# Kernel tuning notes

Hardware: AMD Instinct MI355X
Metric: run time of the kernel (lower is better)

Reference implementation:

```python
import jax, jax.numpy as jnp
import numpy as np

H = 128          # hidden_dim
L = 3            # num_layers
EPS = 1e-5       # BatchNorm eps


def setup_inputs() -> dict:
    key = jax.random.key(0)
    ks = jax.random.split(key, 12)
    B, N = 32, 8192
    s = 0.05
    x = jax.random.normal(ks[0], (B, N, 2), dtype=jnp.float32)
    mask = jnp.ones((B, N), dtype=jnp.float32)
    # parameters, stored as [in, out]
    emb_w = jax.random.normal(ks[1], (2, H), jnp.float32) * s
    emb_b = jnp.zeros((H,), jnp.float32)
    lin_w = jax.random.normal(ks[2], (L, H, H), jnp.float32) * s
    lin_b = jnp.zeros((L, H), jnp.float32)
    nb_w = jax.random.normal(ks[3], (L, H, H), jnp.float32) * s
    nb_b = jnp.zeros((L, H), jnp.float32)
    bn_g = jnp.ones((L, H), jnp.float32)
    bn_b = jnp.zeros((L, H), jnp.float32)
    out1_w = jax.random.normal(ks[4], (H, H // 2), jnp.float32) * s
    out1_b = jnp.zeros((H // 2,), jnp.float32)
    out2_w = jax.random.normal(ks[5], (H // 2, 2), jnp.float32) * s
    out2_b = jnp.zeros((2,), jnp.float32)
    return dict(x=x, mask=mask, emb_w=emb_w, emb_b=emb_b,
                lin_w=lin_w, lin_b=lin_b, nb_w=nb_w, nb_b=nb_b,
                bn_g=bn_g, bn_b=bn_b, out1_w=out1_w, out1_b=out1_b,
                out2_w=out2_w, out2_b=out2_b)


def reference(x, mask, emb_w, emb_b, lin_w, lin_b, nb_w, nb_b,
              bn_g, bn_b, out1_w, out1_b, out2_w, out2_b):
    m = mask[..., None]                     # [B, N, 1]
    h = x @ emb_w + emb_b                   # [B, N, H]
    for i in range(L):
        # graph conv: self transform + ring-neighbor (roll) transform
        nsum = jnp.roll(h, 1, axis=1) + jnp.roll(h, -1, axis=1)
        h_new = (h @ lin_w[i] + lin_b[i] + nsum @ nb_w[i] + nb_b[i]) * m
        # BatchNorm1d (training-mode batch stats over batch*nodes per channel)
        mean = jnp.mean(h_new, axis=(0, 1))
        var = jnp.mean(jnp.square(h_new - mean), axis=(0, 1))  # biased var
        h_new = (h_new - mean) * jax.lax.rsqrt(var + EPS) * bn_g[i] + bn_b[i]
        h_new = jax.nn.relu(h_new)          # dropout treated as identity (eval)
        h = h + h_new                       # residual
    out = jax.nn.relu(h @ out1_w + out1_b) @ out2_w + out2_b  # [B, N, 2]
    return out * m
```

## Files before the change

kernel.cpp:

```cpp
#include <hip/hip_runtime.h>
#include <cstddef>

#define H      128
#define NBATCH 32
#define NN     8192
#define RTOT   (NBATCH*NN)
#define NLAYER 3
#define BNEPS  1e-5f
#define NSLOT  16
#define CNPB   128
#define HNPB   64
#define HS_STRIDE 136

typedef _Float16 f16;
typedef __attribute__((ext_vector_type(8))) _Float16 half8;
typedef __attribute__((ext_vector_type(4))) float f32x4;

__device__ __forceinline__ void unpackh8(uint4 pk, float* d) {
    const f16* hp = (const f16*)&pk;
    #pragma unroll
    for (int i = 0; i < 8; ++i) d[i] = (float)hp[i];
}
__device__ __forceinline__ uint4 packh8(const float* s) {
    uint4 pk;
    f16* hp = (f16*)&pk;
    #pragma unroll
    for (int i = 0; i < 8; ++i) hp[i] = (f16)s[i];
    return pk;
}

__device__ __forceinline__ void load_bfrags(
    const f16* __restrict__ Wt, half8 bW[2][4], int colbase, int l15, int quad)
{
    #pragma unroll
    for (int nt = 0; nt < 2; ++nt) {
        int nrow = colbase + nt * 16 + l15;
        #pragma unroll
        for (int ks = 0; ks < 4; ++ks)
            bW[nt][ks] = *((const half8*)(Wt + nrow * 128 + ks * 32 + quad * 8));
    }
}

__device__ __forceinline__ void conv_mfma8(
    const f16* __restrict__ hs, const half8 bWl[2][4], const half8 bWn[2][4],
    f32x4 acc[8][2], int l15, int quad)
{
    #pragma unroll
    for (int mt = 0; mt < 8; ++mt) {
        acc[mt][0] = (f32x4){0.f, 0.f, 0.f, 0.f};
        acc[mt][1] = (f32x4){0.f, 0.f, 0.f, 0.f};
    }
    #pragma unroll
    for (int ks = 0; ks < 4; ++ks) {
        #pragma unroll
        for (int mt = 0; mt < 8; ++mt) {
            int row = mt * 16 + l15;
            const f16* base = hs + row * HS_STRIDE + ks * 32 + quad * 8;
            half8 hm = *((const half8*)(base + HS_STRIDE));
            half8 hd = *((const half8*)(base));
            half8 hu = *((const half8*)(base + 2 * HS_STRIDE));
            half8 an = hd + hu;
            acc[mt][0] = __builtin_amdgcn_mfma_f32_16x16x32_f16(hm, bWl[0][ks], acc[mt][0], 0, 0, 0);
            acc[mt][1] = __builtin_amdgcn_mfma_f32_16x16x32_f16(hm, bWl[1][ks], acc[mt][1], 0, 0, 0);
            acc[mt][0] = __builtin_amdgcn_mfma_f32_16x16x32_f16(an, bWn[0][ks], acc[mt][0], 0, 0, 0);
            acc[mt][1] = __builtin_amdgcn_mfma_f32_16x16x32_f16(an, bWn[1][ks], acc[mt][1], 0, 0, 0);
        }
    }
}

__global__ __launch_bounds__(256) void k_prep(
    const float* __restrict__ lin_w, const float* __restrict__ nb_w,
    f16* __restrict__ Wlt, f16* __restrict__ Wnt)
{
    int id = blockIdx.x * 256 + threadIdx.x;
    int mat = id / 49152;
    int r   = id - mat * 49152;
    int l   = r >> 14;
    int r2  = r & 16383;
    int k   = r2 >> 7;
    int n   = r2 & 127;
    const float* src = mat ? nb_w : lin_w;
    f16*         dst = mat ? Wnt  : Wlt;
    dst[l * 16384 + n * 128 + k] = (f16)src[l * 16384 + k * 128 + n];
}

__device__ __forceinline__ void conv_epilogue(
    f32x4 acc[8][2], const float bsum[2], const float* __restrict__ msk,
    f16* __restrict__ tr, f16* __restrict__ hnb, float* __restrict__ gstats,
    int r0, int colbase, int l15, int quad, int lane, int t, int slot)
{
    float s[2] = {0.f, 0.f}, ss[2] = {0.f, 0.f};
    #pragma unroll
    for (int nt = 0; nt < 2; ++nt) {
        int col = colbase + nt * 16 + l15;
        #pragma unroll
        for (int mt = 0; mt < 8; ++mt)
            #pragma unroll
            for (int reg = 0; reg < 4; ++reg) {
                int lrow = mt * 16 + quad * 4 + reg;
                float v = (acc[mt][nt][reg] + bsum[nt]) * msk[lrow];
                tr[lrow * HS_STRIDE + col] = (f16)v;
                s[nt] += v; ss[nt] += v * v;
            }
    }
    #pragma unroll
    for (int nt = 0; nt < 2; ++nt) {
        s[nt]  += __shfl_xor(s[nt], 16);  s[nt]  += __shfl_xor(s[nt], 32);
        ss[nt] += __shfl_xor(ss[nt], 16); ss[nt] += __shfl_xor(ss[nt], 32);
    }
    if (lane < 16)
        #pragma unroll
        for (int nt = 0; nt < 2; ++nt) {
            int col = colbase + nt * 16 + lane;
            atomicAdd(&gstats[slot * 2 * H + col],     s[nt]);
            atomicAdd(&gstats[slot * 2 * H + H + col], ss[nt]);
        }
    __syncthreads();
    for (int i = t; i < CNPB * 16; i += 256) {
        int row = i >> 4, g = i & 15;
        *((uint4*)(hnb + (size_t)(r0 + row) * H + g * 8)) =
            *((const uint4*)(tr + row * HS_STRIDE + g * 8));
    }
}

__global__ __launch_bounds__(256) void k_conv0f(
    const float* __restrict__ x, const float* __restrict__ ew,
    const float* __restrict__ eb,
    const f16* __restrict__ Wlt, const f16* __restrict__ Wnt,
    const float* __restrict__ bl, const float* __restrict__ bnb,
    const float* __restrict__ mask,
    f16* __restrict__ hnb, float* __restrict__ gstats)
{
    __shared__ __align__(16) f16 smem[(CNPB + 2) * HS_STRIDE];
    __shared__ float ews[3 * H], msk[CNPB];
    f16* hs = smem;
    f16* tr = smem;
    const int t = threadIdx.x, lane = t & 63;
    const int l15 = lane & 15, quad = lane >> 4;
    const int colbase = (t >> 6) * 32;
    const int r0 = blockIdx.x * CNPB;
    const int batch = r0 >> 13, n0 = r0 & (NN - 1);

    half8 bWl[2][4], bWn[2][4];
    load_bfrags(Wlt, bWl, colbase, l15, quad);
    load_bfrags(Wnt, bWn, colbase, l15, quad);
    float bsum[2];
    #pragma unroll
    for (int nt = 0; nt < 2; ++nt) {
        int col = colbase + nt * 16 + l15;
        bsum[nt] = bl[col] + bnb[col];
    }
    for (int c = t; c < H; c += 256) {
        ews[c] = ew[c]; ews[H + c] = ew[H + c]; ews[2 * H + c] = eb[c];
    }
    if (t < CNPB) msk[t] = mask[r0 + t];
    __syncthreads();

    for (int i = t; i < (CNPB + 2) * 16; i += 256) {
        int row = i >> 4, g = i & 15;
        int n = (n0 + row - 1 + NN) & (NN - 1);
        const float* xp = x + 2 * ((size_t)batch * NN + n);
        float x0 = xp[0], x1 = xp[1];
        f16 o[8];
        #pragma unroll
        for (int e = 0; e < 8; ++e) {
            int c = g * 8 + e;
            o[e] = (f16)fmaf(x1, ews[H + c], fmaf(x0, ews[c], ews[2 * H + c]));
        }
        *((uint4*)(hs + row * HS_STRIDE + g * 8)) = *((const uint4*)o);
    }
    __syncthreads();

    f32x4 acc[8][2];
    conv_mfma8(hs, bWl, bWn, acc, l15, quad);
    __syncthreads();

    conv_epilogue(acc, bsum, msk, tr, hnb, gstats,
                  r0, colbase, l15, quad, lane, t, blockIdx.x & (NSLOT - 1));
}

__global__ __launch_bounds__(256) void k_conv(
    const f16* __restrict__ hb,
    const f16* __restrict__ Wlt, const f16* __restrict__ Wnt,
    const float* __restrict__ bl, const float* __restrict__ bnb,
    const float* __restrict__ mask,
    f16* __restrict__ hnb, float* __restrict__ gstats)
{
    __shared__ __align__(16) f16 smem[(CNPB + 2) * HS_STRIDE];
    __shared__ float msk[CNPB];
    f16* hs = smem;
    f16* tr = smem;
    const int t = threadIdx.x, lane = t & 63;
    const int l15 = lane & 15, quad = lane >> 4;
    const int colbase = (t >> 6) * 32;
    const int r0 = blockIdx.x * CNPB;
    const int batch = r0 >> 13, n0 = r0 & (NN - 1);

    half8 bWl[2][4], bWn[2][4];
    load_bfrags(Wlt, bWl, colbase, l15, quad);
    load_bfrags(Wnt, bWn, colbase, l15, quad);
    float bsum[2];
    #pragma unroll
    for (int nt = 0; nt < 2; ++nt) {
        int col = colbase + nt * 16 + l15;
        bsum[nt] = bl[col] + bnb[col];
    }
    if (t < CNPB) msk[t] = mask[r0 + t];

    for (int i = t; i < (CNPB + 2) * 16; i += 256) {
        int row = i >> 4, g = i & 15;
        int n = (n0 + row - 1 + NN) & (NN - 1);
        *((uint4*)(hs + row * HS_STRIDE + g * 8)) =
            *((const uint4*)(hb + ((size_t)(batch * NN + n)) * H + g * 8));
    }
    __syncthreads();

    f32x4 acc[8][2];
    conv_mfma8(hs, bWl, bWn, acc, l15, quad);
    __syncthreads();

    conv_epilogue(acc, bsum, msk, tr, hnb, gstats,
                  r0, colbase, l15, quad, lane, t, blockIdx.x & (NSLOT - 1));
}

__global__ __launch_bounds__(256) void k_norm0(
    const float* __restrict__ x, const float* __restrict__ ew,
    const float* __restrict__ eb, const f16* __restrict__ hnb,
    const float* __restrict__ gstats, const float* __restrict__ bn_g,
    const float* __restrict__ bn_b, f16* __restrict__ hb)
{
    __shared__ float scl_s[H], sft_s[H], ews[3 * H];
    const int t = threadIdx.x;
    if (t < H) {
        float s = 0.f, ss = 0.f;
        #pragma unroll
        for (int i = 0; i < NSLOT; ++i) {
            s  += gstats[i * 2 * H + t];
            ss += gstats[i * 2 * H + H + t];
        }
        const float invR = 1.f / (float)RTOT;
        float mean = s * invR;
        float var  = ss * invR - mean * mean;
        float inv  = rsqrtf(var + BNEPS);
        float sc   = bn_g[t] * inv;
        scl_s[t] = sc;
        sft_s[t] = fmaf(-mean, sc, bn_b[t]);
        ews[t] = ew[t]; ews[H + t] = ew[H + t]; ews[2 * H + t] = eb[t];
    }
    __syncthreads();

    for (size_t idx = (size_t)blockIdx.x * 256 + t; idx < (size_t)RTOT * 16;
         idx += (size_t)gridDim.x * 256) {
        size_t row = idx >> 4;
        int g = idx & 15;
        float x0 = x[2 * row], x1 = x[2 * row + 1];
        uint4 pn = *((const uint4*)(hnb + row * H + g * 8));
        float vn[8], vh[8];
        unpackh8(pn, vn);
        #pragma unroll
        for (int e = 0; e < 8; ++e) {
            int c = g * 8 + e;
            float h0 = fmaf(x1, ews[H + c], fmaf(x0, ews[c], ews[2 * H + c]));
            vh[e] = h0 + fmaxf(fmaf(vn[e], scl_s[c], sft_s[c]), 0.f);
        }
        *((uint4*)(hb + row * H + g * 8)) = packh8(vh);
    }
}

__global__ __launch_bounds__(256) void k_norm(
    const f16* __restrict__ hnb, const float* __restrict__ gstats,
    const float* __restrict__ bn_g, const float* __restrict__ bn_b,
    f16* __restrict__ hb)
{
    __shared__ float scl_s[H], sft_s[H];
    const int t = threadIdx.x;
    if (t < H) {
        float s = 0.f, ss = 0.f;
        #pragma unroll
        for (int i = 0; i < NSLOT; ++i) {
            s  += gstats[i * 2 * H + t];
            ss += gstats[i * 2 * H + H + t];
        }
        const float invR = 1.f / (float)RTOT;
        float mean = s * invR;
        float var  = ss * invR - mean * mean;
        float inv  = rsqrtf(var + BNEPS);
        float sc   = bn_g[t] * inv;
        scl_s[t] = sc;
        sft_s[t] = fmaf(-mean, sc, bn_b[t]);
    }
    __syncthreads();

    for (size_t idx = (size_t)blockIdx.x * 256 + t; idx < (size_t)RTOT * 16;
         idx += (size_t)gridDim.x * 256) {
        size_t row = idx >> 4;
        int g = idx & 15;
        uint4 pn = *((const uint4*)(hnb + row * H + g * 8));
        uint4 ph = *((const uint4*)(hb  + row * H + g * 8));
        float vn[8], vh[8];
        unpackh8(pn, vn);
        unpackh8(ph, vh);
        #pragma unroll
        for (int e = 0; e < 8; ++e) {
            int c = g * 8 + e;
            vh[e] += fmaxf(fmaf(vn[e], scl_s[c], sft_s[c]), 0.f);
        }
        *((uint4*)(hb + row * H + g * 8)) = packh8(vh);
    }
}

__global__ __launch_bounds__(256) void k_head(
    const f16* __restrict__ hb, const float* __restrict__ W1,
    const float* __restrict__ b1, const float* __restrict__ W2,
    const float* __restrict__ b2, const float* __restrict__ mask,
    float* __restrict__ out)
{
    __shared__ f16 hs [64 * HS_STRIDE];
    __shared__ f16 w1t[64 * HS_STRIDE];
    const int t    = threadIdx.x;
    const int wave = t >> 6;
    const int lane = t & 63;
    const int l15  = lane & 15;
    const int quad = lane >> 4;
    const int r0   = blockIdx.x * HNPB;

    for (int i = t; i < 64 * 16; i += 256) {
        int row = i >> 4, g = i & 15;
        *((uint4*)(hs + row * HS_STRIDE + g * 8)) =
            *((const uint4*)(hb + (size_t)(r0 + row) * H + g * 8));
    }
    for (int i = t; i < H * 64; i += 256) {
        int k = i >> 6, n = i & 63;
        w1t[n * HS_STRIDE + k] = (f16)W1[i];
    }
    __syncthreads();

    f32x4 acc[4];
    #pragma unroll
    for (int nt = 0; nt < 4; ++nt) acc[nt] = (f32x4){0.f, 0.f, 0.f, 0.f};

    #pragma unroll
    for (int ks = 0; ks < 4; ++ks) {
        half8 a = *((const half8*)(hs + (wave * 16 + l15) * HS_STRIDE + ks * 32 + quad * 8));
        #pragma unroll
        for (int nt = 0; nt < 4; ++nt) {
            half8 b = *((const half8*)(w1t + (nt * 16 + l15) * HS_STRIDE + ks * 32 + quad * 8));
            acc[nt] = __builtin_amdgcn_mfma_f32_16x16x32_f16(a, b, acc[nt], 0, 0, 0);
        }
    }

    float p0[4] = {0,0,0,0}, p1[4] = {0,0,0,0};
    #pragma unroll
    for (int nt = 0; nt < 4; ++nt) {
        int col = nt * 16 + l15;
        float bb = b1[col];
        float wa = W2[2 * col], wb = W2[2 * col + 1];
        #pragma unroll
        for (int reg = 0; reg < 4; ++reg) {
            float v = fmaxf(acc[nt][reg] + bb, 0.f);
            p0[reg] = fmaf(v, wa, p0[reg]);
            p1[reg] = fmaf(v, wb, p1[reg]);
        }
    }
    #pragma unroll
    for (int reg = 0; reg < 4; ++reg) {
        p0[reg] += __shfl_xor(p0[reg], 1); p0[reg] += __shfl_xor(p0[reg], 2);
        p0[reg] += __shfl_xor(p0[reg], 4); p0[reg] += __shfl_xor(p0[reg], 8);
        p1[reg] += __shfl_xor(p1[reg], 1); p1[reg] += __shfl_xor(p1[reg], 2);
        p1[reg] += __shfl_xor(p1[reg], 4); p1[reg] += __shfl_xor(p1[reg], 8);
    }
    if (l15 == 0) {
        #pragma unroll
        for (int reg = 0; reg < 4; ++reg) {
            int gr = r0 + wave * 16 + quad * 4 + reg;
            float m = mask[gr];
            float2 o;
            o.x = (p0[reg] + b2[0]) * m;
            o.y = (p1[reg] + b2[1]) * m;
            *((float2*)(out + 2 * gr)) = o;
        }
    }
}

extern "C" void kernel_launch(void* const* d_in, const int* in_sizes, int n_in,
                              void* d_out, int out_size, void* d_ws, size_t ws_size,
                              hipStream_t stream)
{
    const float* x     = (const float*)d_in[0];
    const float* mask  = (const float*)d_in[1];
    const float* emb_w = (const float*)d_in[2];
    const float* emb_b = (const float*)d_in[3];
    const float* lin_w = (const float*)d_in[4];
    const float* lin_b = (const float*)d_in[5];
    const float* nb_w  = (const float*)d_in[6];
    const float* nb_b  = (const float*)d_in[7];
    const float* bn_g  = (const float*)d_in[8];
    const float* bn_b  = (const float*)d_in[9];
    const float* o1w   = (const float*)d_in[10];
    const float* o1b   = (const float*)d_in[11];
    const float* o2w   = (const float*)d_in[12];
    const float* o2b   = (const float*)d_in[13];
    float* out = (float*)d_out;

    char* ws = (char*)d_ws;
    f16* hb  = (f16*)ws;
    f16* hnb = (f16*)(ws + (size_t)RTOT * H * 2);

    float* gst = (float*)d_out;
    f16* Wlt = (f16*)((float*)d_out + 65536);
    f16* Wnt = Wlt + NLAYER * H * H;

    hipMemsetAsync(gst, 0, NLAYER * NSLOT * 2 * H * sizeof(float), stream);
    k_prep<<<384, 256, 0, stream>>>(lin_w, nb_w, Wlt, Wnt);

    k_conv0f<<<RTOT / CNPB, 256, 0, stream>>>(
        x, emb_w, emb_b, Wlt, Wnt, lin_b, nb_b, mask, hnb, gst);
    k_norm0<<<2048, 256, 0, stream>>>(
        x, emb_w, emb_b, hnb, gst, bn_g, bn_b, hb);

    for (int i = 1; i < NLAYER; ++i) {
        k_conv<<<RTOT / CNPB, 256, 0, stream>>>(
            hb, Wlt + i * H * H, Wnt + i * H * H,
            lin_b + i * H, nb_b + i * H, mask,
            hnb, gst + i * NSLOT * 2 * H);
        k_norm<<<2048, 256, 0, stream>>>(
            hnb, gst + i * NSLOT * 2 * H, bn_g + i * H, bn_b + i * H, hb);
    }
    k_head<<<RTOT / HNPB, 256, 0, stream>>>(hb, o1w, o1b, o2w, o2b, mask, out);
}
```

Measured before the change: 352.6 us.

## Store conv output in MFMA fragment order and transpose in norm kernels

The conv epilogue now writes each wave's accumulator fragments straight to global memory in a fragment-native blocked layout. This drops the shared-memory transpose and its two block barriers. The norm kernels now run one block per 128-row tile, read that blocked layout coalesced, apply BN and ReLU, and scatter into shared memory to transpose back to row-major before the residual add. This moves transpose work from the conv kernel to the norm kernel and adds scattered 2-byte LDS stores there, which may cause bank conflicts.

```diff
diff --git a/kernel.cpp b/kernel.cpp
--- a/kernel.cpp
+++ b/kernel.cpp
@@ -84,42 +84,42 @@
     dst[l * 16384 + n * 128 + k] = (f16)src[l * 16384 + k * 128 + n];
 }
 
-__device__ __forceinline__ void conv_epilogue(
+__device__ __forceinline__ void conv_epilogue_c(
     f32x4 acc[8][2], const float bsum[2], const float* __restrict__ msk,
-    f16* __restrict__ tr, f16* __restrict__ hnb, float* __restrict__ gstats,
-    int r0, int colbase, int l15, int quad, int lane, int t, int slot)
-{
+    f16* __restrict__ hnb, float* __restrict__ gstats,
+    int blk, int wave, int quad, int lane, int slot)
+{
+    uint2* out2 = (uint2*)hnb;
     float s[2] = {0.f, 0.f}, ss[2] = {0.f, 0.f};
     #pragma unroll
     for (int nt = 0; nt < 2; ++nt) {
-        int col = colbase + nt * 16 + l15;
-        #pragma unroll
-        for (int mt = 0; mt < 8; ++mt)
+        #pragma unroll
+        for (int mt = 0; mt < 8; ++mt) {
+            f16 v4[4];
             #pragma unroll
             for (int reg = 0; reg < 4; ++reg) {
                 int lrow = mt * 16 + quad * 4 + reg;
                 float v = (acc[mt][nt][reg] + bsum[nt]) * msk[lrow];
-                tr[lrow * HS_STRIDE + col] = (f16)v;
+                v4[reg] = (f16)v;
                 s[nt] += v; ss[nt] += v * v;
             }
+            size_t chunk = ((size_t)blk * 4 + wave) * 16 + mt * 2 + nt;
+            out2[chunk * 64 + lane] = *((const uint2*)v4);
+        }
     }
     #pragma unroll
     for (int nt = 0; nt < 2; ++nt) {
         s[nt]  += __shfl_xor(s[nt], 16);  s[nt]  += __shfl_xor(s[nt], 32);
         ss[nt] += __shfl_xor(ss[nt], 16); ss[nt] += __shfl_xor(ss[nt], 32);
     }
-    if (lane < 16)
+    if (lane < 16) {
+        int colbase = wave * 32;
         #pragma unroll
         for (int nt = 0; nt < 2; ++nt) {
             int col = colbase + nt * 16 + lane;
             atomicAdd(&gstats[slot * 2 * H + col],     s[nt]);
             atomicAdd(&gstats[slot * 2 * H + H + col], ss[nt]);
         }
-    __syncthreads();
-    for (int i = t; i < CNPB * 16; i += 256) {
-        int row = i >> 4, g = i & 15;
-        *((uint4*)(hnb + (size_t)(r0 + row) * H + g * 8)) =
-            *((const uint4*)(tr + row * HS_STRIDE + g * 8));
     }
 }
 
@@ -131,13 +131,12 @@
     const float* __restrict__ mask,
     f16* __restrict__ hnb, float* __restrict__ gstats)
 {
-    __shared__ __align__(16) f16 smem[(CNPB + 2) * HS_STRIDE];
+    __shared__ __align__(16) f16 hs[(CNPB + 2) * HS_STRIDE];
     __shared__ float ews[3 * H], msk[CNPB];
-    f16* hs = smem;
-    f16* tr = smem;
     const int t = threadIdx.x, lane = t & 63;
     const int l15 = lane & 15, quad = lane >> 4;
-    const int colbase = (t >> 6) * 32;
+    const int wave = t >> 6;
+    const int colbase = wave * 32;
     const int r0 = blockIdx.x * CNPB;
     const int batch = r0 >> 13, n0 = r0 & (NN - 1);
 
@@ -173,10 +172,9 @@
 
     f32x4 acc[8][2];
     conv_mfma8(hs, bWl, bWn, acc, l15, quad);
-    __syncthreads();
-
-    conv_epilogue(acc, bsum, msk, tr, hnb, gstats,
-                  r0, colbase, l15, quad, lane, t, blockIdx.x & (NSLOT - 1));
+
+    conv_epilogue_c(acc, bsum, msk, hnb, gstats,
+                    blockIdx.x, wave, quad, lane, blockIdx.x & (NSLOT - 1));
 }
 
 __global__ __launch_bounds__(256) void k_conv(
@@ -186,13 +184,12 @@
     const float* __restrict__ mask,
     f16* __restrict__ hnb, float* __restrict__ gstats)
 {
-    __shared__ __align__(16) f16 smem[(CNPB + 2) * HS_STRIDE];
+    __shared__ __align__(16) f16 hs[(CNPB + 2) * HS_STRIDE];
     __shared__ float msk[CNPB];
-    f16* hs = smem;
-    f16* tr = smem;
     const int t = threadIdx.x, lane = t & 63;
     const int l15 = lane & 15, quad = lane >> 4;
-    const int colbase = (t >> 6) * 32;
+    const int wave = t >> 6;
+    const int colbase = wave * 32;
     const int r0 = blockIdx.x * CNPB;
     const int batch = r0 >> 13, n0 = r0 & (NN - 1);
 
@@ -217,20 +214,42 @@
 
     f32x4 acc[8][2];
     conv_mfma8(hs, bWl, bWn, acc, l15, quad);
-    __syncthreads();
-
-    conv_epilogue(acc, bsum, msk, tr, hnb, gstats,
-                  r0, colbase, l15, quad, lane, t, blockIdx.x & (NSLOT - 1));
-}
-
-__global__ __launch_bounds__(256) void k_norm0(
-    const float* __restrict__ x, const float* __restrict__ ew,
-    const float* __restrict__ eb, const f16* __restrict__ hnb,
+
+    conv_epilogue_c(acc, bsum, msk, hnb, gstats,
+                    blockIdx.x, wave, quad, lane, blockIdx.x & (NSLOT - 1));
+}
+
+__device__ __forceinline__ void norm_ingest(
+    const f16* __restrict__ hnb, int blk, int t,
+    const float* __restrict__ scl_s, const float* __restrict__ sft_s,
+    f16* __restrict__ g)
+{
+    const uint4* src = (const uint4*)hnb + (size_t)blk * 2048;
+    for (int i = t; i < 2048; i += 256) {
+        uint4 pk = src[i];
+        int chunk = i >> 5;
+        int L     = (i & 31) * 2;
+        int ntv   = chunk & 1;
+        int mtv   = (chunk >> 1) & 7;
+        int wv    = chunk >> 4;
+        int c0    = wv * 32 + ntv * 16 + (L & 15);
+        int row0  = mtv * 16 + (L >> 4) * 4;
+        float vv[8];
+        unpackh8(pk, vv);
+        #pragma unroll
+        for (int e = 0; e < 8; ++e) {
+            int cc = c0 + (e >> 2);
+            int rr = row0 + (e & 3);
+            float q = fmaxf(fmaf(vv[e], scl_s[cc], sft_s[cc]), 0.f);
+            g[rr * HS_STRIDE + cc] = (f16)q;
+        }
+    }
+}
+
+__device__ __forceinline__ void bn_finalize(
     const float* __restrict__ gstats, const float* __restrict__ bn_g,
-    const float* __restrict__ bn_b, f16* __restrict__ hb)
-{
-    __shared__ float scl_s[H], sft_s[H], ews[3 * H];
-    const int t = threadIdx.x;
+    const float* __restrict__ bn_b, int t, float* scl_s, float* sft_s)
+{
     if (t < H) {
         float s = 0.f, ss = 0.f;
         #pragma unroll
@@ -245,25 +264,42 @@
         float sc   = bn_g[t] * inv;
         scl_s[t] = sc;
         sft_s[t] = fmaf(-mean, sc, bn_b[t]);
-        ews[t] = ew[t]; ews[H + t] = ew[H + t]; ews[2 * H + t] = eb[t];
-    }
-    __syncthreads();
-
-    for (size_t idx = (size_t)blockIdx.x * 256 + t; idx < (size_t)RTOT * 16;
-         idx += (size_t)gridDim.x * 256) {
-        size_t row = idx >> 4;
-        int g = idx & 15;
-        float x0 = x[2 * row], x1 = x[2 * row + 1];
-        uint4 pn = *((const uint4*)(hnb + row * H + g * 8));
-        float vn[8], vh[8];
-        unpackh8(pn, vn);
+    }
+}
+
+__global__ __launch_bounds__(256) void k_norm0(
+    const float* __restrict__ x, const float* __restrict__ ew,
+    const float* __restrict__ eb, const f16* __restrict__ hnb,
+    const float* __restrict__ gstats, const float* __restrict__ bn_g,
+    const float* __restrict__ bn_b, f16* __restrict__ hb)
+{
+    __shared__ __align__(16) f16 g[CNPB * HS_STRIDE];
+    __shared__ float scl_s[H], sft_s[H], ews[3 * H];
+    const int t = threadIdx.x;
+    const int blk = blockIdx.x;
+    const size_t r0 = (size_t)blk * CNPB;
+
+    bn_finalize(gstats, bn_g, bn_b, t, scl_s, sft_s);
+    if (t < H) { ews[t] = ew[t]; ews[H + t] = ew[H + t]; ews[2 * H + t] = eb[t]; }
+    __syncthreads();
+
+    norm_ingest(hnb, blk, t, scl_s, sft_s, g);
+    __syncthreads();
+
+    for (int i = t; i < 2048; i += 256) {
+        int row = i >> 4, gg = i & 15;
+        size_t grow = r0 + row;
+        float x0 = x[2 * grow], x1 = x[2 * grow + 1];
+        uint4 pg = *((const uint4*)(g + row * HS_STRIDE + gg * 8));
+        float vg[8], vh[8];
+        unpackh8(pg, vg);
         #pragma unroll
         for (int e = 0; e < 8; ++e) {
-            int c = g * 8 + e;
+            int c = gg * 8 + e;
             float h0 = fmaf(x1, ews[H + c], fmaf(x0, ews[c], ews[2 * H + c]));
-            vh[e] = h0 + fmaxf(fmaf(vn[e], scl_s[c], sft_s[c]), 0.f);
-        }
-        *((uint4*)(hb + row * H + g * 8)) = packh8(vh);
+            vh[e] = h0 + vg[e];
+        }
+        *((uint4*)(hb + grow * H + gg * 8)) = packh8(vh);
     }
 }
 
@@ -272,40 +308,29 @@
     const float* __restrict__ bn_g, const float* __restrict__ bn_b,
     f16* __restrict__ hb)
 {
+    __shared__ __align__(16) f16 g[CNPB * HS_STRIDE];
     __shared__ float scl_s[H], sft_s[H];
     const int t = threadIdx.x;
-    if (t < H) {
-        float s = 0.f, ss = 0.f;
-        #pragma unroll
-        for (int i = 0; i < NSLOT; ++i) {
-            s  += gstats[i * 2 * H + t];
-            ss += gstats[i * 2 * H + H + t];
-        }
-        const float invR = 1.f / (float)RTOT;
-        float mean = s * invR;
-        float var  = ss * invR - mean * mean;
-        float inv  = rsqrtf(var + BNEPS);
-        float sc   = bn_g[t] * inv;
-        scl_s[t] = sc;
-        sft_s[t] = fmaf(-mean, sc, bn_b[t]);
-    }
-    __syncthreads();
-
-    for (size_t idx = (size_t)blockIdx.x * 256 + t; idx < (size_t)RTOT * 16;
-         idx += (size_t)gridDim.x * 256) {
-        size_t row = idx >> 4;
-        int g = idx & 15;
-        uint4 pn = *((const uint4*)(hnb + row * H + g * 8));
-        uint4 ph = *((const uint4*)(hb  + row * H + g * 8));
-        float vn[8], vh[8];
-        unpackh8(pn, vn);
+    const int blk = blockIdx.x;
+    const size_t r0 = (size_t)blk * CNPB;
+
+    bn_finalize(gstats, bn_g, bn_b, t, scl_s, sft_s);
+    __syncthreads();
+
+    norm_ingest(hnb, blk, t, scl_s, sft_s, g);
+    __syncthreads();
+
+    for (int i = t; i < 2048; i += 256) {
+        int row = i >> 4, gg = i & 15;
+        size_t grow = r0 + row;
+        uint4 ph = *((const uint4*)(hb + grow * H + gg * 8));
+        uint4 pg = *((const uint4*)(g + row * HS_STRIDE + gg * 8));
+        float vh[8], vg[8];
         unpackh8(ph, vh);
-        #pragma unroll
-        for (int e = 0; e < 8; ++e) {
-            int c = g * 8 + e;
-            vh[e] += fmaxf(fmaf(vn[e], scl_s[c], sft_s[c]), 0.f);
-        }
-        *((uint4*)(hb + row * H + g * 8)) = packh8(vh);
+        unpackh8(pg, vg);
+        #pragma unroll
+        for (int e = 0; e < 8; ++e) vh[e] += vg[e];
+        *((uint4*)(hb + grow * H + gg * 8)) = packh8(vh);
     }
 }
 
@@ -415,7 +440,7 @@
 
     k_conv0f<<<RTOT / CNPB, 256, 0, stream>>>(
         x, emb_w, emb_b, Wlt, Wnt, lin_b, nb_b, mask, hnb, gst);
-    k_norm0<<<2048, 256, 0, stream>>>(
+    k_norm0<<<RTOT / CNPB, 256, 0, stream>>>(
         x, emb_w, emb_b, hnb, gst, bn_g, bn_b, hb);
 
     for (int i = 1; i < NLAYER; ++i) {
@@ -423,7 +448,7 @@
             hb, Wlt + i * H * H, Wnt + i * H * H,
             lin_b + i * H, nb_b + i * H, mask,
             hnb, gst + i * NSLOT * 2 * H);
-        k_norm<<<2048, 256, 0, stream>>>(
+        k_norm<<<RTOT / CNPB, 256, 0, stream>>>(
             hnb, gst + i * NSLOT * 2 * H, bn_g + i * H, bn_b + i * H, hb);
     }
     k_head<<<RTOT / HNPB, 256, 0, stream>>>(hb, o1w, o1b, o2w, o2b, mask, out);
```

Measured after the change: 342.9 us. -2.8%, faster.
